# Performance work log

Hardware: AMD Instinct MI355X
Metric: run time of the kernel (lower is better)

## Reference

```python
import jax, jax.numpy as jnp
import numpy as np

N_NODES = 100000
N_EDGES = 1600000
H_DIM = 64  # pos(32) + vel(32)


def _mlp_init(key, d_in, d_hid, d_out):
    k1, k2 = jax.random.split(key)
    s1 = 1.0 / np.sqrt(d_in)
    s2 = 1.0 / np.sqrt(d_hid)
    w1 = jax.random.uniform(k1, (d_in, d_hid), jnp.float32, -s1, s1)
    w2 = jax.random.uniform(k2, (d_hid, d_out), jnp.float32, -s2, s2)
    return w1, jnp.zeros((d_hid,), jnp.float32), w2, jnp.zeros((d_out,), jnp.float32)


def setup_inputs() -> dict:
    key = jax.random.key(0)
    ks = jax.random.split(key, 6)
    pos = jax.random.normal(ks[0], (N_NODES, 32), jnp.float32)
    vel = jax.random.normal(ks[1], (N_NODES, 32), jnp.float32)
    edge_index = jax.random.randint(ks[2], (2, N_EDGES), 0, N_NODES, jnp.int32)
    msg_w1, msg_b1, msg_w2, msg_b2 = _mlp_init(ks[3], 2 * H_DIM, 64, 64)
    upd_w1, upd_b1, upd_w2, upd_b2 = _mlp_init(ks[4], H_DIM + 64, 64, 64)
    sp = 1.0 / np.sqrt(64)
    pred_w = jax.random.uniform(ks[5], (64, 32), jnp.float32, -sp, sp)
    pred_b = jnp.zeros((32,), jnp.float32)
    return dict(pos=pos, vel=vel, edge_index=edge_index,
                msg_w1=msg_w1, msg_b1=msg_b1, msg_w2=msg_w2, msg_b2=msg_b2,
                upd_w1=upd_w1, upd_b1=upd_b1, upd_w2=upd_w2, upd_b2=upd_b2,
                pred_w=pred_w, pred_b=pred_b)


def reference(pos, vel, edge_index,
              msg_w1, msg_b1, msg_w2, msg_b2,
              upd_w1, upd_b1, upd_w2, upd_b2,
              pred_w, pred_b):
    n = pos.shape[0]
    h = jnp.concatenate([pos, vel], axis=-1)              # [N, 64]
    src, dst = edge_index[0], edge_index[1]
    h_i = h[dst]                                          # [E, 64] target nodes
    h_j = h[src]                                          # [E, 64] source nodes
    # message MLP on concat(h_i, h_j)
    m = jnp.concatenate([h_i, h_j], axis=-1)              # [E, 128]
    m = jax.nn.relu(m @ msg_w1 + msg_b1) @ msg_w2 + msg_b2  # [E, 64]
    # scatter-add aggregate to target nodes
    aggr = jax.ops.segment_sum(m, dst, num_segments=n)    # [N, 64]
    # update MLP on concat(h, aggr)
    u = jnp.concatenate([h, aggr], axis=-1)               # [N, 128]
    u = jax.nn.relu(u @ upd_w1 + upd_b1) @ upd_w2 + upd_b2  # [N, 64]
    # linear prediction head -> acceleration
    return u @ pred_w + pred_b                            # [N, 32]
```

## Files before the change

### kernel.cpp

```cpp
#include <hip/hip_runtime.h>

#define NN 100000
#define NE 1600000
#define SB   391
#define NBKT 391
#define EPB  4096

typedef _Float16 f16x8 __attribute__((ext_vector_type(8)));
typedef float    f32x4 __attribute__((ext_vector_type(4)));

#define ZB   1563
#define PHB  3125
#define PWB  13

extern "C" __global__ void __launch_bounds__(256)
prep_kernel(const float* __restrict__ pos, const float* __restrict__ vel,
            const int* __restrict__ ei,
            const float* __restrict__ mw1, const float* __restrict__ mw2,
            const float* __restrict__ uw1, const float* __restrict__ uw2,
            const float* __restrict__ pw,
            _Float16* __restrict__ hh,
            _Float16* __restrict__ mw1f, _Float16* __restrict__ mw2f,
            _Float16* __restrict__ uw1f, _Float16* __restrict__ uw2f,
            _Float16* __restrict__ pwf,
            float* __restrict__ aggr, int* __restrict__ cntm)
{
    __shared__ int lh[NBKT];
    const int b = blockIdx.x, tid = threadIdx.x;
    if (b < ZB) {
        float4* p = (float4*)aggr;
        const int base4 = b * 1024 + tid;
        const float4 z = make_float4(0.f, 0.f, 0.f, 0.f);
#pragma unroll
        for (int k = 0; k < 4; ++k) {
            const int idx = base4 + k * 256;
            if (idx < NN * 16) p[idx] = z;
        }
    } else if (b < ZB + PHB) {
        const int t = (b - ZB) * 256 + tid;
        const int node = t >> 3, seg = t & 7;
        const float* src = (seg < 4) ? pos + (size_t)node * 32 + seg * 8
                                     : vel + (size_t)node * 32 + (seg - 4) * 8;
        const float4 a = ((const float4*)src)[0];
        const float4 c = ((const float4*)src)[1];
        f16x8 r;
        r[0]=(_Float16)a.x; r[1]=(_Float16)a.y; r[2]=(_Float16)a.z; r[3]=(_Float16)a.w;
        r[4]=(_Float16)c.x; r[5]=(_Float16)c.y; r[6]=(_Float16)c.z; r[7]=(_Float16)c.w;
        *(f16x8*)(hh + (size_t)node * 64 + seg * 8) = r;
    } else if (b < ZB + PHB + PWB) {
        const int t2 = (b - ZB - PHB) * 256 + tid;
        if (t2 < 1024) {
            const int t = t2 >> 8, kk = (t2 >> 6) & 3, l = t2 & 63;
            f16x8 r;
#pragma unroll
            for (int j = 0; j < 8; ++j)
                r[j] = (_Float16)mw1[(kk * 32 + (l >> 4) * 8 + j) * 64 + t * 16 + (l & 15)];
            *(f16x8*)(mw1f + (size_t)t2 * 8) = r;
        } else if (t2 < 1536) {
            const int i = t2 - 1024;
            const int t = i >> 7, kk = (i >> 6) & 1, l = i & 63;
            f16x8 r;
#pragma unroll
            for (int j = 0; j < 8; ++j)
                r[j] = (_Float16)mw2[(kk * 32 + (l >> 4) * 8 + j) * 64 + t * 16 + (l & 15)];
            *(f16x8*)(mw2f + (size_t)i * 8) = r;
        } else if (t2 < 2560) {
            const int i = t2 - 1536;
            const int t = i >> 8, kk = (i >> 6) & 3, l = i & 63;
            f16x8 r;
#pragma unroll
            for (int j = 0; j < 8; ++j)
                r[j] = (_Float16)uw1[(kk * 32 + (l >> 4) * 8 + j) * 64 + t * 16 + (l & 15)];
            *(f16x8*)(uw1f + (size_t)i * 8) = r;
        } else if (t2 < 3072) {
            const int i = t2 - 2560;
            const int t = i >> 7, kk = (i >> 6) & 1, l = i & 63;
            f16x8 r;
#pragma unroll
            for (int j = 0; j < 8; ++j)
                r[j] = (_Float16)uw2[(kk * 32 + (l >> 4) * 8 + j) * 64 + t * 16 + (l & 15)];
            *(f16x8*)(uw2f + (size_t)i * 8) = r;
        } else if (t2 < 3328) {
            const int i = t2 - 3072;
            const int t = i >> 7, kk = (i >> 6) & 1, l = i & 63;
            f16x8 r;
#pragma unroll
            for (int j = 0; j < 8; ++j)
                r[j] = (_Float16)pw[(kk * 32 + (l >> 4) * 8 + j) * 32 + t * 16 + (l & 15)];
            *(f16x8*)(pwf + (size_t)i * 8) = r;
        }
    } else {
        const int blk = b - (ZB + PHB + PWB);
        for (int i = tid; i < NBKT; i += 256) lh[i] = 0;
        __syncthreads();
        const int e0 = blk * EPB;
#pragma unroll
        for (int k = 0; k < EPB / 256; ++k) {
            const int e = e0 + k * 256 + tid;
            if (e < NE) atomicAdd(&lh[ei[NE + e] >> 8], 1);
        }
        __syncthreads();
        for (int i = tid; i < NBKT; i += 256) cntm[blk * NBKT + i] = lh[i];
    }
}

extern "C" __global__ void __launch_bounds__(512)
scancol_kernel(const int* __restrict__ cntm, int* __restrict__ offs,
               int* __restrict__ btot)
{
    __shared__ int s[512];
    const int tid = threadIdx.x, bkt = blockIdx.x;
    const int v = (tid < SB) ? cntm[tid * NBKT + bkt] : 0;
    s[tid] = v;
    __syncthreads();
    for (int off = 1; off < 512; off <<= 1) {
        int t = (tid >= off) ? s[tid - off] : 0;
        __syncthreads();
        s[tid] += t;
        __syncthreads();
    }
    if (tid < SB) offs[tid * NBKT + bkt] = s[tid] - v;
    if (tid == SB - 1) btot[bkt] = s[tid];
}

extern "C" __global__ void __launch_bounds__(512)
scanb_kernel(const int* __restrict__ btot, int* __restrict__ bbase)
{
    __shared__ int s[512];
    const int tid = threadIdx.x;
    const int v = (tid < NBKT) ? btot[tid] : 0;
    s[tid] = v;
    __syncthreads();
    for (int off = 1; off < 512; off <<= 1) {
        int t = (tid >= off) ? s[tid - off] : 0;
        __syncthreads();
        s[tid] += t;
        __syncthreads();
    }
    if (tid < NBKT) bbase[tid] = s[tid] - v;
    if (tid == NBKT - 1) bbase[NBKT] = s[tid];
}

extern "C" __global__ void __launch_bounds__(256)
sortC_kernel(const int* __restrict__ ei, const int* __restrict__ offs,
             const int* __restrict__ bbase, int2* __restrict__ sd_tmp)
{
    __shared__ int lh[NBKT];
    __shared__ int lo[NBKT];
    const int tid = threadIdx.x, blk = blockIdx.x;
    for (int i = tid; i < NBKT; i += 256) {
        lh[i] = 0;
        lo[i] = bbase[i] + offs[blk * NBKT + i];
    }
    __syncthreads();
    const int e0 = blk * EPB;
#pragma unroll
    for (int k = 0; k < EPB / 256; ++k) {
        const int e = e0 + k * 256 + tid;
        if (e < NE) {
            const int s = ei[e], d = ei[NE + e];
            const int bkt = d >> 8;
            const int r = atomicAdd(&lh[bkt], 1);
            sd_tmp[lo[bkt] + r] = make_int2(s, d);
        }
    }
}

extern "C" __global__ void __launch_bounds__(256)
sortD_kernel(const int2* __restrict__ sd_tmp, const int* __restrict__ bbase,
             int2* __restrict__ sd2)
{
    __shared__ int h[256];
    __shared__ int s[256];
    __shared__ int dbase[256];
    const int tid = threadIdx.x, bkt = blockIdx.x;
    const int s0 = bbase[bkt], s1 = bbase[bkt + 1];
    const int n = s1 - s0;
    h[tid] = 0;
    __syncthreads();
    for (int k = tid; k < n; k += 256)
        atomicAdd(&h[sd_tmp[s0 + k].y & 255], 1);
    __syncthreads();
    const int v = h[tid];
    s[tid] = v;
    __syncthreads();
    for (int off = 1; off < 256; off <<= 1) {
        int t = (tid >= off) ? s[tid - off] : 0;
        __syncthreads();
        s[tid] += t;
        __syncthreads();
    }
    dbase[tid] = s[tid] - v;
    __syncthreads();
    h[tid] = 0;
    __syncthreads();
    for (int k = tid; k < n; k += 256) {
        const int2 e = sd_tmp[s0 + k];
        const int dl = e.y & 255;
        const int r = atomicAdd(&h[dl], 1);
        sd2[s0 + dbase[dl] + r] = e;
    }
}

extern "C" __global__ void __launch_bounds__(512, 4)
edgeagg_kernel(const _Float16* __restrict__ hh,
               const int2* __restrict__ sd,
               const _Float16* __restrict__ w1f, const _Float16* __restrict__ w2f,
               const float* __restrict__ b1, const float* __restrict__ b2,
               float* __restrict__ aggr)
{
    __shared__ _Float16 sW1[4 * 4 * 64 * 8];
    __shared__ _Float16 sW2[4 * 2 * 64 * 8];
    __shared__ _Float16 sT[8][16 * 64];

    const int tid = threadIdx.x;
    const int wave = tid >> 6, lane = tid & 63;
    const int m = lane & 15, g = lane >> 4;
    const int wslot = (blockIdx.x * 8 + wave) * 64;

    const int2 sdv = sd[wslot + lane];

    const int prevd = __shfl_up(sdv.y, 1, 64);
    const unsigned long long bmask = __ballot(lane == 0 || sdv.y != prevd);

    {
        const uint4* g1 = (const uint4*)w1f; uint4* s1 = (uint4*)sW1;
#pragma unroll
        for (int i = 0; i < 2; ++i) s1[i * 512 + tid] = g1[i * 512 + tid];
        const uint4* g2 = (const uint4*)w2f; uint4* s2 = (uint4*)sW2;
        s2[tid] = g2[tid];
    }

    const float bb1[4] = { b1[m], b1[16 + m], b1[32 + m], b1[48 + m] };
    const float bb2[4] = { b2[m], b2[16 + m], b2[32 + m], b2[48 + m] };

    __syncthreads();

    _Float16* Y = sT[wave];

    float racc = 0.0f;
    int   rnode = __builtin_amdgcn_readlane(sdv.y, 0);
    int   firstRun = 1;

    f16x8 Abuf[2][4];
    {
        const int ns = __shfl(sdv.x, m, 64);
        const int nd = __shfl(sdv.y, m, 64);
        const _Float16* hd = hh + (size_t)nd * 64 + g * 8;
        const _Float16* hs = hh + (size_t)ns * 64 + g * 8;
        Abuf[0][0] = *(const f16x8*)(hd);
        Abuf[0][1] = *(const f16x8*)(hd + 32);
        Abuf[0][2] = *(const f16x8*)(hs);
        Abuf[0][3] = *(const f16x8*)(hs + 32);
    }

#pragma unroll
    for (int it = 0; it < 4; ++it) {
        const int cur = it & 1;
        if (it < 3) {
            const int ns = __shfl(sdv.x, (it + 1) * 16 + m, 64);
            const int nd = __shfl(sdv.y, (it + 1) * 16 + m, 64);
            const _Float16* hd = hh + (size_t)nd * 64 + g * 8;
            const _Float16* hs = hh + (size_t)ns * 64 + g * 8;
            Abuf[cur ^ 1][0] = *(const f16x8*)(hd);
            Abuf[cur ^ 1][1] = *(const f16x8*)(hd + 32);
            Abuf[cur ^ 1][2] = *(const f16x8*)(hs);
            Abuf[cur ^ 1][3] = *(const f16x8*)(hs + 32);
        }

        f32x4 acc[4] = {};
#pragma unroll
        for (int t = 0; t < 4; ++t) {
#pragma unroll
            for (int kk = 0; kk < 4; ++kk) {
                const f16x8 b = *(const f16x8*)(sW1 + ((t * 4 + kk) * 64 + lane) * 8);
                acc[t] = __builtin_amdgcn_mfma_f32_16x16x32_f16(Abuf[cur][kk], b, acc[t], 0, 0, 0);
            }
        }

#pragma unroll
        for (int t = 0; t < 4; ++t) {
#pragma unroll
            for (int r = 0; r < 4; ++r) {
                const float y = fmaxf(acc[t][r] + bb1[t], 0.0f);
                const int row = g * 4 + r, col = t * 16 + m;
                const int byteoff = row * 128 + ((2 * col) ^ ((row & 7) << 4));
                *(_Float16*)((char*)Y + byteoff) = (_Float16)y;
            }
        }
        asm volatile("s_waitcnt lgkmcnt(0)" ::: "memory");
        __builtin_amdgcn_sched_barrier(0);

        f16x8 a2[2];
#pragma unroll
        for (int kk = 0; kk < 2; ++kk) {
            const int c = kk * 4 + g;
            a2[kk] = *(const f16x8*)((char*)Y + m * 128 + ((c * 16) ^ ((m & 7) << 4)));
        }
        asm volatile("s_waitcnt lgkmcnt(0)" ::: "memory");
        __builtin_amdgcn_sched_barrier(0);

        f32x4 acc2[4] = {};
#pragma unroll
        for (int kk = 0; kk < 2; ++kk) {
#pragma unroll
            for (int t = 0; t < 4; ++t) {
                const f16x8 b = *(const f16x8*)(sW2 + ((t * 2 + kk) * 64 + lane) * 8);
                acc2[t] = __builtin_amdgcn_mfma_f32_16x16x32_f16(a2[kk], b, acc2[t], 0, 0, 0);
            }
        }
#pragma unroll
        for (int t = 0; t < 4; ++t)
#pragma unroll
            for (int r = 0; r < 4; ++r) acc2[t][r] += bb2[t];

        const unsigned tm = (unsigned)((bmask >> (it * 16)) & 0xFFFFull) | 0x10000u;
        if (tm == 0x10000u) {
            float p0 = 0.f, p1 = 0.f, p2 = 0.f, p3 = 0.f;
#pragma unroll
            for (int r = 0; r < 4; ++r) {
                p0 += acc2[0][r]; p1 += acc2[1][r];
                p2 += acc2[2][r]; p3 += acc2[3][r];
            }
            p0 += __shfl_xor(p0, 16); p0 += __shfl_xor(p0, 32);
            p1 += __shfl_xor(p1, 16); p1 += __shfl_xor(p1, 32);
            p2 += __shfl_xor(p2, 16); p2 += __shfl_xor(p2, 32);
            p3 += __shfl_xor(p3, 16); p3 += __shfl_xor(p3, 32);
            racc += (g == 0) ? p0 : (g == 1) ? p1 : (g == 2) ? p2 : p3;
        } else {
            int a = 0;
            while (a < 16) {
                const int b = a + 1 + __builtin_ctz(tm >> (a + 1));
                const int d = __builtin_amdgcn_readlane(sdv.y, it * 16 + a);
                if (d != rnode) {
                    float* ap = aggr + (size_t)rnode * 64 + lane;
                    if (firstRun) atomicAdd(ap, racc);
                    else          *ap = racc;
                    firstRun = 0; racc = 0.0f; rnode = d;
                }
                float p0 = 0.f, p1 = 0.f, p2 = 0.f, p3 = 0.f;
#pragma unroll
                for (int r = 0; r < 4; ++r) {
                    const int rowl = 4 * g + r;
                    const bool in = (rowl >= a) && (rowl < b);
                    p0 += in ? acc2[0][r] : 0.f;
                    p1 += in ? acc2[1][r] : 0.f;
                    p2 += in ? acc2[2][r] : 0.f;
                    p3 += in ? acc2[3][r] : 0.f;
                }
                p0 += __shfl_xor(p0, 16); p0 += __shfl_xor(p0, 32);
                p1 += __shfl_xor(p1, 16); p1 += __shfl_xor(p1, 32);
                p2 += __shfl_xor(p2, 16); p2 += __shfl_xor(p2, 32);
                p3 += __shfl_xor(p3, 16); p3 += __shfl_xor(p3, 32);
                racc += (g == 0) ? p0 : (g == 1) ? p1 : (g == 2) ? p2 : p3;
                a = b;
            }
        }
    }
    atomicAdd(aggr + (size_t)rnode * 64 + lane, racc);
}

extern "C" __global__ void __launch_bounds__(256)
node_mfma_kernel(const _Float16* __restrict__ hh, const float* __restrict__ aggr,
                 const _Float16* __restrict__ uw1f, const _Float16* __restrict__ uw2f,
                 const _Float16* __restrict__ pwf,
                 const float* __restrict__ b1, const float* __restrict__ b2,
                 const float* __restrict__ pb, float* __restrict__ out)
{
    __shared__ _Float16 sU1[4 * 4 * 64 * 8];
    __shared__ _Float16 sU2[4 * 2 * 64 * 8];
    __shared__ _Float16 sPW[2 * 2 * 64 * 8];
    __shared__ _Float16 sT[4][16 * 64];

    const int tid = threadIdx.x;
    {
        const uint4* g1 = (const uint4*)uw1f; uint4* s1 = (uint4*)sU1;
#pragma unroll
        for (int i = 0; i < 4; ++i) s1[i * 256 + tid] = g1[i * 256 + tid];
        const uint4* g2 = (const uint4*)uw2f; uint4* s2 = (uint4*)sU2;
#pragma unroll
        for (int i = 0; i < 2; ++i) s2[i * 256 + tid] = g2[i * 256 + tid];
        const uint4* g3 = (const uint4*)pwf;  uint4* s3 = (uint4*)sPW;
        s3[tid] = g3[tid];
    }
    __syncthreads();

    const int wave = tid >> 6, lane = tid & 63;
    const int m = lane & 15, g = lane >> 4;
    const int nb = (blockIdx.x * 4 + wave) * 16;
    const int v = nb + m;
    const int vl = (v < NN) ? v : (NN - 1);

    const _Float16* hv = hh + (size_t)vl * 64 + g * 8;
    const f16x8 a0 = *(const f16x8*)(hv);
    const f16x8 a1 = *(const f16x8*)(hv + 32);
    const float* av = aggr + (size_t)vl * 64 + g * 8;
    const float4 x0 = *(const float4*)(av),      x1 = *(const float4*)(av + 4);
    const float4 y0 = *(const float4*)(av + 32), y1 = *(const float4*)(av + 36);
    f16x8 a2, a3;
    a2[0]=(_Float16)x0.x; a2[1]=(_Float16)x0.y; a2[2]=(_Float16)x0.z; a2[3]=(_Float16)x0.w;
    a2[4]=(_Float16)x1.x; a2[5]=(_Float16)x1.y; a2[6]=(_Float16)x1.z; a2[7]=(_Float16)x1.w;
    a3[0]=(_Float16)y0.x; a3[1]=(_Float16)y0.y; a3[2]=(_Float16)y0.z; a3[3]=(_Float16)y0.w;
    a3[4]=(_Float16)y1.x; a3[5]=(_Float16)y1.y; a3[6]=(_Float16)y1.z; a3[7]=(_Float16)y1.w;

    f32x4 acc[4] = {};
#pragma unroll
    for (int t = 0; t < 4; ++t) {
        acc[t] = __builtin_amdgcn_mfma_f32_16x16x32_f16(
            a0, *(const f16x8*)(sU1 + ((t * 4 + 0) * 64 + lane) * 8), acc[t], 0, 0, 0);
        acc[t] = __builtin_amdgcn_mfma_f32_16x16x32_f16(
            a1, *(const f16x8*)(sU1 + ((t * 4 + 1) * 64 + lane) * 8), acc[t], 0, 0, 0);
        acc[t] = __builtin_amdgcn_mfma_f32_16x16x32_f16(
            a2, *(const f16x8*)(sU1 + ((t * 4 + 2) * 64 + lane) * 8), acc[t], 0, 0, 0);
        acc[t] = __builtin_amdgcn_mfma_f32_16x16x32_f16(
            a3, *(const f16x8*)(sU1 + ((t * 4 + 3) * 64 + lane) * 8), acc[t], 0, 0, 0);
    }

    _Float16* Y = sT[wave];
#pragma unroll
    for (int t = 0; t < 4; ++t) {
        const float bb = b1[t * 16 + m];
#pragma unroll
        for (int r = 0; r < 4; ++r) {
            const float y = fmaxf(acc[t][r] + bb, 0.0f);
            const int row = g * 4 + r, col = t * 16 + m;
            const int byteoff = row * 128 + ((2 * col) ^ ((row & 7) << 4));
            *(_Float16*)((char*)Y + byteoff) = (_Float16)y;
        }
    }
    asm volatile("s_waitcnt lgkmcnt(0)" ::: "memory");
    __builtin_amdgcn_sched_barrier(0);

    f16x8 ay[2];
#pragma unroll
    for (int kk = 0; kk < 2; ++kk) {
        const int c = kk * 4 + g;
        ay[kk] = *(const f16x8*)((char*)Y + m * 128 + ((c * 16) ^ ((m & 7) << 4)));
    }
    asm volatile("s_waitcnt lgkmcnt(0)" ::: "memory");
    __builtin_amdgcn_sched_barrier(0);

    f32x4 acc2[4] = {};
#pragma unroll
    for (int kk = 0; kk < 2; ++kk) {
#pragma unroll
        for (int t = 0; t < 4; ++t) {
            const f16x8 b = *(const f16x8*)(sU2 + ((t * 2 + kk) * 64 + lane) * 8);
            acc2[t] = __builtin_amdgcn_mfma_f32_16x16x32_f16(ay[kk], b, acc2[t], 0, 0, 0);
        }
    }

#pragma unroll
    for (int t = 0; t < 4; ++t) {
        const float bb = b2[t * 16 + m];
#pragma unroll
        for (int r = 0; r < 4; ++r) {
            const float u = acc2[t][r] + bb;
            const int row = g * 4 + r, col = t * 16 + m;
            const int byteoff = row * 128 + ((2 * col) ^ ((row & 7) << 4));
            *(_Float16*)((char*)Y + byteoff) = (_Float16)u;
        }
    }
    asm volatile("s_waitcnt lgkmcnt(0)" ::: "memory");
    __builtin_amdgcn_sched_barrier(0);

    f16x8 au[2];
#pragma unroll
    for (int kk = 0; kk < 2; ++kk) {
        const int c = kk * 4 + g;
        au[kk] = *(const f16x8*)((char*)Y + m * 128 + ((c * 16) ^ ((m & 7) << 4)));
    }
    asm volatile("s_waitcnt lgkmcnt(0)" ::: "memory");
    __builtin_amdgcn_sched_barrier(0);

    f32x4 acc3[2] = {};
#pragma unroll
    for (int kk = 0; kk < 2; ++kk) {
#pragma unroll
        for (int t = 0; t < 2; ++t) {
            const f16x8 b = *(const f16x8*)(sPW + ((t * 2 + kk) * 64 + lane) * 8);
            acc3[t] = __builtin_amdgcn_mfma_f32_16x16x32_f16(au[kk], b, acc3[t], 0, 0, 0);
        }
    }

    float* F = (float*)Y;
#pragma unroll
    for (int t = 0; t < 2; ++t) {
        const float bb = pb[t * 16 + m];
#pragma unroll
        for (int r = 0; r < 4; ++r) {
            const int row = g * 4 + r, col = t * 16 + m;
            const int byteoff = row * 128 + ((4 * col) ^ ((row & 7) << 4));
            *(float*)((char*)F + byteoff) = acc3[t][r] + bb;
        }
    }
    asm volatile("s_waitcnt lgkmcnt(0)" ::: "memory");
    __builtin_amdgcn_sched_barrier(0);

    const int row = lane >> 2, q = lane & 3;
    const float4 o0 = *(const float4*)((char*)F + row * 128 + ((q * 16)       ^ ((row & 7) << 4)));
    const float4 o1 = *(const float4*)((char*)F + row * 128 + (((q + 4) * 16) ^ ((row & 7) << 4)));
    if (nb + row < NN) {
        float4* op = (float4*)(out + (size_t)(nb + row) * 32);
        op[q]     = o0;
        op[q + 4] = o1;
    }
}

extern "C" __global__ void __launch_bounds__(256)
edge_msg_kernel(const float* __restrict__ pos, const float* __restrict__ vel,
                const int* __restrict__ ei,
                const float* __restrict__ w1, const float* __restrict__ b1,
                const float* __restrict__ w2, const float* __restrict__ b2,
                float* __restrict__ aggr)
{
    const int e = blockIdx.x * 256 + threadIdx.x;
    if (e >= NE) return;
    const int ns = ei[e];
    const int nd = ei[NE + e];
    float y[64];
#pragma unroll
    for (int j = 0; j < 64; ++j) y[j] = b1[j];
    for (int part = 0; part < 4; ++part) {
        const int    node  = (part < 2) ? nd : ns;
        const float* basep = (part & 1) ? vel : pos;
        const float4* xp = reinterpret_cast<const float4*>(basep + (size_t)node * 32);
        const float*  wp = w1 + part * 32 * 64;
        for (int q = 0; q < 8; ++q) {
            const float4 xv = xp[q];
#pragma unroll
            for (int kk = 0; kk < 4; ++kk) {
                const float xs = (kk == 0) ? xv.x : (kk == 1) ? xv.y
                               : (kk == 2) ? xv.z : xv.w;
                const float* wr = wp + (q * 4 + kk) * 64;
#pragma unroll
                for (int j = 0; j < 64; ++j) y[j] = fmaf(xs, wr[j], y[j]);
            }
        }
    }
    float mm[64];
#pragma unroll
    for (int c = 0; c < 64; ++c) mm[c] = b2[c];
#pragma unroll
    for (int j = 0; j < 64; ++j) {
        const float yj = fmaxf(y[j], 0.0f);
        const float* wr = w2 + j * 64;
#pragma unroll
        for (int c = 0; c < 64; ++c) mm[c] = fmaf(yj, wr[c], mm[c]);
    }
    float* ap = aggr + (size_t)nd * 64;
#pragma unroll
    for (int c = 0; c < 64; ++c) atomicAdd(ap + c, mm[c]);
}

extern "C" __global__ void __launch_bounds__(256)
node_upd_kernel(const float* __restrict__ pos, const float* __restrict__ vel,
                const float* __restrict__ aggr,
                const float* __restrict__ w1, const float* __restrict__ b1,
                const float* __restrict__ w2, const float* __restrict__ b2,
                const float* __restrict__ pw, const float* __restrict__ pb,
                float* __restrict__ out)
{
    const int v = blockIdx.x * 256 + threadIdx.x;
    if (v >= NN) return;

    float y[64];
#pragma unroll
    for (int j = 0; j < 64; ++j) y[j] = b1[j];
    for (int part = 0; part < 4; ++part) {
        const float* basep = (part == 0) ? pos + (size_t)v * 32
                           : (part == 1) ? vel + (size_t)v * 32
                           : aggr + (size_t)v * 64 + (size_t)(part - 2) * 32;
        const float4* xp = reinterpret_cast<const float4*>(basep);
        const float*  wp = w1 + part * 32 * 64;
        for (int q = 0; q < 8; ++q) {
            const float4 xv = xp[q];
#pragma unroll
            for (int kk = 0; kk < 4; ++kk) {
                const float xs = (kk == 0) ? xv.x : (kk == 1) ? xv.y
                               : (kk == 2) ? xv.z : xv.w;
                const float* wr = wp + (q * 4 + kk) * 64;
#pragma unroll
                for (int j = 0; j < 64; ++j) y[j] = fmaf(xs, wr[j], y[j]);
            }
        }
    }

    float u[64];
#pragma unroll
    for (int c = 0; c < 64; ++c) u[c] = b2[c];
#pragma unroll
    for (int j = 0; j < 64; ++j) {
        const float yj = fmaxf(y[j], 0.0f);
        const float* wr = w2 + j * 64;
#pragma unroll
        for (int c = 0; c < 64; ++c) u[c] = fmaf(yj, wr[c], u[c]);
    }

    float o[32];
#pragma unroll
    for (int c = 0; c < 32; ++c) o[c] = pb[c];
#pragma unroll
    for (int j = 0; j < 64; ++j) {
        const float* wr = pw + j * 32;
#pragma unroll
        for (int c = 0; c < 32; ++c) o[c] = fmaf(u[j], wr[c], o[c]);
    }

    float4* op = reinterpret_cast<float4*>(out + (size_t)v * 32);
#pragma unroll
    for (int q = 0; q < 8; ++q)
        op[q] = make_float4(o[q * 4], o[q * 4 + 1], o[q * 4 + 2], o[q * 4 + 3]);
}

extern "C" void kernel_launch(void* const* d_in, const int* in_sizes, int n_in,
                              void* d_out, int out_size, void* d_ws, size_t ws_size,
                              hipStream_t stream)
{
    const float* pos = (const float*)d_in[0];
    const float* vel = (const float*)d_in[1];
    const int*   ei  = (const int*)d_in[2];
    const float* mw1 = (const float*)d_in[3];
    const float* mb1 = (const float*)d_in[4];
    const float* mw2 = (const float*)d_in[5];
    const float* mb2 = (const float*)d_in[6];
    const float* uw1 = (const float*)d_in[7];
    const float* ub1 = (const float*)d_in[8];
    const float* uw2 = (const float*)d_in[9];
    const float* ub2 = (const float*)d_in[10];
    const float* pw  = (const float*)d_in[11];
    const float* pb  = (const float*)d_in[12];
    float* out = (float*)d_out;

    char* ws = (char*)d_ws;
    size_t off = 0;
    float*    aggr   = (float*)(ws + off);    off += (size_t)NN * 64 * 4;
    _Float16* hh     = (_Float16*)(ws + off); off += (size_t)NN * 64 * 2;
    int2*     sd_tmp = (int2*)(ws + off);     off += (size_t)NE * 8;
    int2*     sd2    = (int2*)(ws + off);     off += (size_t)NE * 8;
    int*      cntm   = (int*)(ws + off);      off += (size_t)SB * NBKT * 4;
    int*      offs   = (int*)(ws + off);      off += (size_t)SB * NBKT * 4;
    int*      btot   = (int*)(ws + off);      off += 512 * 4;
    int*      bbase  = (int*)(ws + off);      off += 512 * 4;
    _Float16* mw1f   = (_Float16*)(ws + off); off += 1024 * 8 * 2;
    _Float16* mw2f   = (_Float16*)(ws + off); off += 512 * 8 * 2;
    _Float16* uw1f   = (_Float16*)(ws + off); off += 1024 * 8 * 2;
    _Float16* uw2f   = (_Float16*)(ws + off); off += 512 * 8 * 2;
    _Float16* pwf    = (_Float16*)(ws + off); off += 256 * 8 * 2;
    const size_t need_full = off;

    if (ws_size >= need_full) {
        prep_kernel<<<ZB + PHB + PWB + SB, 256, 0, stream>>>(
            pos, vel, ei, mw1, mw2, uw1, uw2, pw,
            hh, mw1f, mw2f, uw1f, uw2f, pwf, aggr, cntm);
        scancol_kernel<<<NBKT, 512, 0, stream>>>(cntm, offs, btot);
        scanb_kernel<<<1, 512, 0, stream>>>(btot, bbase);
        sortC_kernel<<<SB, 256, 0, stream>>>(ei, offs, bbase, sd_tmp);
        sortD_kernel<<<NBKT, 256, 0, stream>>>(sd_tmp, bbase, sd2);
        edgeagg_kernel<<<NE / 512, 512, 0, stream>>>(
            hh, sd2, mw1f, mw2f, mb1, mb2, aggr);
        node_mfma_kernel<<<(NN + 63) / 64, 256, 0, stream>>>(
            hh, aggr, uw1f, uw2f, pwf, ub1, ub2, pb, out);
    } else {
        float* aggr2 = (float*)d_ws;
        hipMemsetAsync(aggr2, 0, (size_t)NN * 64 * sizeof(float), stream);
        edge_msg_kernel<<<NE / 256, 256, 0, stream>>>(pos, vel, ei,
                                                      mw1, mb1, mw2, mb2, aggr2);
        node_upd_kernel<<<(NN + 255) / 256, 256, 0, stream>>>(
            pos, vel, aggr2, uw1, ub1, uw2, ub2, pw, pb, out);
    }
}
```

Measured before the change: 137.2 us.

## Merge bucket-base scan into column scan via atomics; simplify edge-MLP LDS staging

Removes the single-block bucket-base scan kernel. Each column-scan block now claims its bucket's base offset with an atomicAdd on a global counter, and sortD reads the bucket size directly. Buckets become contiguous but no longer ordered by index, and a memset of the counter is added to the stream. In the edge MLP kernel the XOR-swizzled LDS staging is replaced by a padded 72-stride layout, biases are folded into the MFMA accumulator initialisation, and the explicit lgkmcnt waits are dropped.

```diff
diff --git a/kernel.cpp b/kernel.cpp
--- a/kernel.cpp
+++ b/kernel.cpp
@@ -105,8 +105,9 @@
 }
 
 extern "C" __global__ void __launch_bounds__(512)
-scancol_kernel(const int* __restrict__ cntm, int* __restrict__ offs,
-               int* __restrict__ btot)
+scancol_kernel(const int* __restrict__ cntm, int* __restrict__ gtot,
+               int* __restrict__ offs, int* __restrict__ btot,
+               int* __restrict__ bbase)
 {
     __shared__ int s[512];
     const int tid = threadIdx.x, bkt = blockIdx.x;
@@ -120,25 +121,11 @@
         __syncthreads();
     }
     if (tid < SB) offs[tid * NBKT + bkt] = s[tid] - v;
-    if (tid == SB - 1) btot[bkt] = s[tid];
-}
-
-extern "C" __global__ void __launch_bounds__(512)
-scanb_kernel(const int* __restrict__ btot, int* __restrict__ bbase)
-{
-    __shared__ int s[512];
-    const int tid = threadIdx.x;
-    const int v = (tid < NBKT) ? btot[tid] : 0;
-    s[tid] = v;
-    __syncthreads();
-    for (int off = 1; off < 512; off <<= 1) {
-        int t = (tid >= off) ? s[tid - off] : 0;
-        __syncthreads();
-        s[tid] += t;
-        __syncthreads();
-    }
-    if (tid < NBKT) bbase[tid] = s[tid] - v;
-    if (tid == NBKT - 1) bbase[NBKT] = s[tid];
+    if (tid == SB - 1) {
+        const int tot = s[tid];
+        btot[bkt]  = tot;
+        bbase[bkt] = atomicAdd(gtot, tot);
+    }
 }
 
 extern "C" __global__ void __launch_bounds__(256)
@@ -168,14 +155,14 @@
 
 extern "C" __global__ void __launch_bounds__(256)
 sortD_kernel(const int2* __restrict__ sd_tmp, const int* __restrict__ bbase,
-             int2* __restrict__ sd2)
+             const int* __restrict__ btot, int2* __restrict__ sd2)
 {
     __shared__ int h[256];
     __shared__ int s[256];
     __shared__ int dbase[256];
     const int tid = threadIdx.x, bkt = blockIdx.x;
-    const int s0 = bbase[bkt], s1 = bbase[bkt + 1];
-    const int n = s1 - s0;
+    const int s0 = bbase[bkt];
+    const int n  = btot[bkt];
     h[tid] = 0;
     __syncthreads();
     for (int k = tid; k < n; k += 256)
@@ -211,7 +198,7 @@
 {
     __shared__ _Float16 sW1[4 * 4 * 64 * 8];
     __shared__ _Float16 sW2[4 * 2 * 64 * 8];
-    __shared__ _Float16 sT[8][16 * 64];
+    __shared__ _Float16 sY[8][16 * 72];
 
     const int tid = threadIdx.x;
     const int wave = tid >> 6, lane = tid & 63;
@@ -219,14 +206,12 @@
     const int wslot = (blockIdx.x * 8 + wave) * 64;
 
     const int2 sdv = sd[wslot + lane];
-
     const int prevd = __shfl_up(sdv.y, 1, 64);
     const unsigned long long bmask = __ballot(lane == 0 || sdv.y != prevd);
 
     {
         const uint4* g1 = (const uint4*)w1f; uint4* s1 = (uint4*)sW1;
-#pragma unroll
-        for (int i = 0; i < 2; ++i) s1[i * 512 + tid] = g1[i * 512 + tid];
+        s1[tid] = g1[tid]; s1[512 + tid] = g1[512 + tid];
         const uint4* g2 = (const uint4*)w2f; uint4* s2 = (uint4*)sW2;
         s2[tid] = g2[tid];
     }
@@ -236,7 +221,9 @@
 
     __syncthreads();
 
-    _Float16* Y = sT[wave];
+    _Float16* Y  = sY[wave];
+    _Float16* Yw = Y + g * 4 * 72 + m;
+    const _Float16* Yr = Y + m * 72 + g * 8;
 
     float racc = 0.0f;
     int   rnode = __builtin_amdgcn_readlane(sdv.y, 0);
@@ -268,7 +255,12 @@
             Abuf[cur ^ 1][3] = *(const f16x8*)(hs + 32);
         }
 
-        f32x4 acc[4] = {};
+        f32x4 acc[4];
+#pragma unroll
+        for (int t = 0; t < 4; ++t) {
+            acc[t][0] = bb1[t]; acc[t][1] = bb1[t];
+            acc[t][2] = bb1[t]; acc[t][3] = bb1[t];
+        }
 #pragma unroll
         for (int t = 0; t < 4; ++t) {
 #pragma unroll
@@ -278,29 +270,25 @@
             }
         }
 
+        __builtin_amdgcn_sched_barrier(0);
 #pragma unroll
         for (int t = 0; t < 4; ++t) {
 #pragma unroll
-            for (int r = 0; r < 4; ++r) {
-                const float y = fmaxf(acc[t][r] + bb1[t], 0.0f);
-                const int row = g * 4 + r, col = t * 16 + m;
-                const int byteoff = row * 128 + ((2 * col) ^ ((row & 7) << 4));
-                *(_Float16*)((char*)Y + byteoff) = (_Float16)y;
-            }
-        }
-        asm volatile("s_waitcnt lgkmcnt(0)" ::: "memory");
+            for (int r = 0; r < 4; ++r)
+                Yw[r * 72 + t * 16] = (_Float16)fmaxf(acc[t][r], 0.0f);
+        }
         __builtin_amdgcn_sched_barrier(0);
 
         f16x8 a2[2];
-#pragma unroll
-        for (int kk = 0; kk < 2; ++kk) {
-            const int c = kk * 4 + g;
-            a2[kk] = *(const f16x8*)((char*)Y + m * 128 + ((c * 16) ^ ((m & 7) << 4)));
-        }
-        asm volatile("s_waitcnt lgkmcnt(0)" ::: "memory");
-        __builtin_amdgcn_sched_barrier(0);
-
-        f32x4 acc2[4] = {};
+        a2[0] = *(const f16x8*)(Yr);
+        a2[1] = *(const f16x8*)(Yr + 32);
+
+        f32x4 acc2[4];
+#pragma unroll
+        for (int t = 0; t < 4; ++t) {
+            acc2[t][0] = bb2[t]; acc2[t][1] = bb2[t];
+            acc2[t][2] = bb2[t]; acc2[t][3] = bb2[t];
+        }
 #pragma unroll
         for (int kk = 0; kk < 2; ++kk) {
 #pragma unroll
@@ -309,10 +297,6 @@
                 acc2[t] = __builtin_amdgcn_mfma_f32_16x16x32_f16(a2[kk], b, acc2[t], 0, 0, 0);
             }
         }
-#pragma unroll
-        for (int t = 0; t < 4; ++t)
-#pragma unroll
-            for (int r = 0; r < 4; ++r) acc2[t][r] += bb2[t];
 
         const unsigned tm = (unsigned)((bmask >> (it * 16)) & 0xFFFFull) | 0x10000u;
         if (tm == 0x10000u) {
@@ -642,6 +626,7 @@
     int*      offs   = (int*)(ws + off);      off += (size_t)SB * NBKT * 4;
     int*      btot   = (int*)(ws + off);      off += 512 * 4;
     int*      bbase  = (int*)(ws + off);      off += 512 * 4;
+    int*      gtot   = (int*)(ws + off);      off += 256;
     _Float16* mw1f   = (_Float16*)(ws + off); off += 1024 * 8 * 2;
     _Float16* mw2f   = (_Float16*)(ws + off); off += 512 * 8 * 2;
     _Float16* uw1f   = (_Float16*)(ws + off); off += 1024 * 8 * 2;
@@ -650,13 +635,13 @@
     const size_t need_full = off;
 
     if (ws_size >= need_full) {
+        hipMemsetAsync(gtot, 0, sizeof(int), stream);
         prep_kernel<<<ZB + PHB + PWB + SB, 256, 0, stream>>>(
             pos, vel, ei, mw1, mw2, uw1, uw2, pw,
             hh, mw1f, mw2f, uw1f, uw2f, pwf, aggr, cntm);
-        scancol_kernel<<<NBKT, 512, 0, stream>>>(cntm, offs, btot);
-        scanb_kernel<<<1, 512, 0, stream>>>(btot, bbase);
+        scancol_kernel<<<NBKT, 512, 0, stream>>>(cntm, gtot, offs, btot, bbase);
         sortC_kernel<<<SB, 256, 0, stream>>>(ei, offs, bbase, sd_tmp);
-        sortD_kernel<<<NBKT, 256, 0, stream>>>(sd_tmp, bbase, sd2);
+        sortD_kernel<<<NBKT, 256, 0, stream>>>(sd_tmp, bbase, btot, sd2);
         edgeagg_kernel<<<NE / 512, 512, 0, stream>>>(
             hh, sd2, mw1f, mw2f, mb1, mb2, aggr);
         node_mfma_kernel<<<(NN + 63) / 64, 256, 0, stream>>>(
```

After: 143.8 us. 4.8% more time.
